# Kernel optimization log

Measured on AMD Instinct MI355X. Metric: run time of the kernel, lower is better.

Reference implementation:

```python
import jax, jax.numpy as jnp
import numpy as np

H = 8      # n_heads
HD = 64    # per-head channels (out_channels in __init__, before *= n_heads)


def setup_inputs() -> dict:
    key = jax.random.key(0)
    ks = jax.random.split(key, 10)
    B, C, N = 4, 256, 2048
    O = H * HD
    s = 1.0 / np.sqrt(C).astype(np.float32)
    return {
        "x": jax.random.normal(ks[0], (B, C, N), dtype=jnp.float32),
        "y": jax.random.normal(ks[1], (B, C, N), dtype=jnp.float32),
        "Wq": jax.random.normal(ks[2], (O, C), dtype=jnp.float32) * s,
        "bq": jnp.zeros((O,), dtype=jnp.float32),
        "Wk": jax.random.normal(ks[3], (O, C), dtype=jnp.float32) * s,
        "bk": jnp.zeros((O,), dtype=jnp.float32),
        "Wv": jax.random.normal(ks[4], (O, C), dtype=jnp.float32) * s,
        "bv": jnp.zeros((O,), dtype=jnp.float32),
        "Wp": jax.random.normal(ks[5], (HD, C), dtype=jnp.float32) * s,  # residual projection, bias=False
        "gamma": jax.random.uniform(ks[6], (H, 1, 1, 1), dtype=jnp.float32) + 0.001,
    }


def _conv1x1(W, b, t):
    # 1x1 Conv1d: (O,C) x (B,C,N) -> (B,O,N)
    out = jnp.einsum('oc,bcn->bon', W, t)
    return out if b is None else out + b[None, :, None]


def _heads(t):
    # (B, H*HD, N) -> (H, B, N, HD); channel split into contiguous per-head chunks
    B, _, N = t.shape
    return t.reshape(B, H, HD, N).transpose(1, 0, 3, 2)


def reference(x, y, Wq, bq, Wk, bk, Wv, bv, Wp, gamma):
    # q/k/v projections via 1x1 convs (kernel_size=1, 'stride_effective' padding => same length)
    q = _heads(_conv1x1(Wq, bq, x))   # (H,B,N,HD)
    k = _heads(_conv1x1(Wk, bk, y))   # (H,B,N,HD)
    v = _heads(_conv1x1(Wv, bv, y))   # (H,B,N,HD)

    # energy = bmm(Q, K^T); softmax over last dim (no mask)
    energy = jnp.einsum('hbnd,hbmd->hbnm', q, k)          # (H,B,N,N)
    attn = jax.nn.softmax(energy, axis=-1)

    # out = bmm(attention.transpose(-2,-1), V)  (note the transpose in the original)
    out = jnp.einsum('hbnm,hbnd->hbmd', attn, v)          # (H,B,N,HD)

    # gamma-weighted residual blend with projected y
    yp = _conv1x1(Wp, None, y).transpose(0, 2, 1)         # (B,N,HD)
    g = gamma.reshape(H, 1, 1, 1)
    out = (g * out + yp[None]) / (1.0 + g)                # (H,B,N,HD)
    return out
```

## Files before the change

### kernel.cpp

```cpp
#include <hip/hip_runtime.h>
#include <math.h>

#define B_DIM 4
#define C_DIM 256
#define N_DIM 2048
#define H_DIM 8
#define HD    64
#define HB    32
#define NTOK  (B_DIM * N_DIM)
#define LOG2E 1.44269504f

typedef __attribute__((ext_vector_type(8))) short bf16x8;
typedef __attribute__((ext_vector_type(4))) float f32x4;

static __device__ __forceinline__ short f2bf(float f) {
    unsigned u = __builtin_bit_cast(unsigned, f);
    u += 0x7fffu + ((u >> 16) & 1u);
    return (short)(u >> 16);
}
static __device__ __forceinline__ float bf2f(short s) {
    unsigned u = ((unsigned)(unsigned short)s) << 16;
    return __builtin_bit_cast(float, u);
}
static __device__ __forceinline__ float fx2(float x) {
#if __has_builtin(__builtin_amdgcn_exp2f)
    return __builtin_amdgcn_exp2f(x);
#else
    return exp2f(x);
#endif
}
static __device__ __forceinline__ unsigned pk_bf16(float a, float b) {
#if __has_builtin(__builtin_amdgcn_cvt_pk_bf16_f32)
    auto v = __builtin_amdgcn_cvt_pk_bf16_f32(a, b);
    return __builtin_bit_cast(unsigned, v);
#else
    unsigned ua = __builtin_bit_cast(unsigned, a);
    unsigned ub = __builtin_bit_cast(unsigned, b);
    return ((ua + 0x8000u) >> 16) | ((ub + 0x8000u) & 0xffff0000u);
#endif
}

#define MFMA16(A, Bv, Cv) __builtin_amdgcn_mfma_f32_16x16x32_bf16(A, Bv, Cv, 0, 0, 0)


__global__ __launch_bounds__(256) void cast_transpose_xy(
    const float* __restrict__ X, const float* __restrict__ Y,
    short* __restrict__ XS, short* __restrict__ YS)
{
    const int z = blockIdx.z;
    const float* src = (z < 4) ? X : Y;
    short* dst = (z < 4) ? XS : YS;
    const int b = z & 3, c0 = blockIdx.y * 64, n0 = blockIdx.x * 64;
    __shared__ float L[64][65];
    const int t = threadIdx.x;
    for (int i = t; i < 4096; i += 256) {
        int cc = i >> 6, nn = i & 63;
        L[cc][nn] = src[((size_t)b * C_DIM + c0 + cc) * N_DIM + n0 + nn];
    }
    __syncthreads();
#pragma unroll
    for (int half = 0; half < 2; ++half) {
        int cid = half * 256 + t;
        int lane = cid & 63, fi = cid >> 6;
        int ksl = fi & 1, rtl = fi >> 1;
        int lo = lane & 15, quad = lane >> 4;
        bf16x8 o;
#pragma unroll
        for (int j = 0; j < 8; ++j) o[j] = f2bf(L[ksl * 32 + quad * 8 + j][rtl * 16 + lo]);
        int rt = b * 128 + (n0 >> 4) + rtl;
        int ks = (c0 >> 5) + ksl;
        *(bf16x8*)(dst + ((size_t)(rt * 8 + ks) * 64 + lane) * 8) = o;
    }
}

__global__ __launch_bounds__(256) void cast_weights(
    const float* __restrict__ Wq, const float* __restrict__ Wk,
    const float* __restrict__ Wv, const float* __restrict__ Wp,
    short* __restrict__ WSx, short* __restrict__ WSy)
{
    int gid = blockIdx.x * 256 + threadIdx.x;
    int lane = gid & 63, chunk = gid >> 6;
    int lo = lane & 15, quad = lane >> 4;
    const float* src; short* dst;
    if (chunk < 256) {
        int ot = chunk >> 3, ks = chunk & 7;
        src = Wq + (size_t)(ot * 16 + lo) * C_DIM + ks * 32 + quad * 8;
        dst = WSx + (size_t)chunk * 512 + lane * 8;
    } else {
        int ch = chunk - 256;
        int ot = ch >> 3, ks = ch & 7;
        int row = ot * 16 + lo;
        const float* base = (row < 512) ? (Wk + (size_t)row * C_DIM)
                          : (row < 1024) ? (Wv + (size_t)(row - 512) * C_DIM)
                                         : (Wp + (size_t)(row - 1024) * C_DIM);
        src = base + ks * 32 + quad * 8;
        dst = WSy + (size_t)ch * 512 + lane * 8;
    }
    bf16x8 o;
#pragma unroll
    for (int j = 0; j < 8; ++j) o[j] = f2bf(src[j]);
    *(bf16x8*)dst = o;
}

__global__ __launch_bounds__(256) void proj_all(
    const short* __restrict__ WSx, const short* __restrict__ WSy,
    const short* __restrict__ XS, const short* __restrict__ YS,
    const float* __restrict__ bq, const float* __restrict__ bk,
    const float* __restrict__ bv,
    short* __restrict__ QS, short* __restrict__ KS,
    short* __restrict__ VSu, float* __restrict__ Yo)
{
    const int oy = blockIdx.y;
    const bool isq = oy < 8;
    const short* WS = isq ? WSx : WSy;
    const short* Xs = isq ? XS : YS;
    const int oyl = isq ? oy : oy - 8;
    const int o0 = oyl * 64;
    const int tok0 = blockIdx.x * 128;
    const int t = threadIdx.x, wave = t >> 6, lane = t & 63;
    const int lo = lane & 15, quad = lane >> 4;

    __shared__ __align__(16) char smem[34816];

    const int ot = oyl * 4 + wave;
    const int rt0 = tok0 >> 4;
    const f32x4 czero = {0.f, 0.f, 0.f, 0.f};

    f32x4 acc[8];
#pragma unroll
    for (int i = 0; i < 8; ++i) acc[i] = czero;

#pragma unroll 2
    for (int ks = 0; ks < 8; ++ks) {
        bf16x8 a = *(const bf16x8*)(WS + ((size_t)(ot * 8 + ks) * 64 + lane) * 8);
#pragma unroll
        for (int nt = 0; nt < 8; ++nt) {
            bf16x8 bx = *(const bf16x8*)(Xs + ((size_t)((rt0 + nt) * 8 + ks) * 64 + lane) * 8);
            acc[nt] = MFMA16(a, bx, acc[nt]);
        }
    }

    const int b = tok0 >> 11;
    const int n0b = tok0 & (N_DIM - 1);

    if (oy < 16) {
        short* T = (short*)smem;
        const float* bias = isq ? bq : bk;
        const float scale = isq ? LOG2E : 1.f;
        float bvr[4];
#pragma unroll
        for (int r = 0; r < 4; ++r) bvr[r] = bias[o0 + wave * 16 + quad * 4 + r];
#pragma unroll
        for (int nt = 0; nt < 8; ++nt) {
            short4 pk;
            pk.x = f2bf((acc[nt][0] + bvr[0]) * scale);
            pk.y = f2bf((acc[nt][1] + bvr[1]) * scale);
            pk.z = f2bf((acc[nt][2] + bvr[2]) * scale);
            pk.w = f2bf((acc[nt][3] + bvr[3]) * scale);
            *(short4*)(T + (nt * 16 + lo) * 72 + wave * 16 + quad * 4) = pk;
        }
        __syncthreads();
        const int h = oyl;
        const int hb = h * 4 + b;
        short* dst = isq ? QS : KS;
#pragma unroll
        for (int s = 0; s < 4; ++s) {
            int cid = s * 256 + t;
            int ln = cid & 63, fi = cid >> 6;
            int ksd = fi & 1, rtl = fi >> 1;
            bf16x8 v = *(const bf16x8*)(T + (rtl * 16 + (ln & 15)) * 72 + ksd * 32 + (ln >> 4) * 8);
            *(bf16x8*)(dst + (((size_t)(hb * 128 + (n0b >> 4) + rtl) * 2 + ksd) * 512 + ln * 8)) = v;
        }
    } else if (oy < 24) {
        short* T2 = (short*)smem;
        float bvr[4];
#pragma unroll
        for (int r = 0; r < 4; ++r) bvr[r] = bv[o0 - 512 + wave * 16 + quad * 4 + r];
#pragma unroll
        for (int nt = 0; nt < 8; ++nt)
#pragma unroll
            for (int r = 0; r < 4; ++r) {
                int ol = wave * 16 + quad * 4 + r;
                T2[ol * 136 + nt * 16 + lo] = f2bf(acc[nt][r] + bvr[r]);
            }
        __syncthreads();
        const int h = oy - 16;
        const int hb = h * 4 + b;
#pragma unroll
        for (int s = 0; s < 4; ++s) {
            int cid = s * 256 + t;
            int ln = cid & 63, fi = cid >> 6;
            int dt = fi & 3, ksd = (fi >> 2) & 1, nbl = fi >> 3;
            int dl = dt * 16 + (ln & 15);
            int tkl = nbl * 64 + ksd * 32 + (ln >> 4) * 8;
            bf16x8 v = *(const bf16x8*)(T2 + dl * 136 + tkl);
            int nbg = (n0b >> 6) + nbl;
            *(bf16x8*)(VSu + ((size_t)(((hb * 32 + nbg) * 2 + ksd) * 4 + dt) * 64 + ln) * 8) = v;
        }
    } else {
        float* T3 = (float*)smem;
#pragma unroll
        for (int nt = 0; nt < 8; ++nt) {
            float4 f;
            f.x = acc[nt][0]; f.y = acc[nt][1]; f.z = acc[nt][2]; f.w = acc[nt][3];
            *(float4*)(T3 + (nt * 16 + lo) * 68 + wave * 16 + quad * 4) = f;
        }
        __syncthreads();
#pragma unroll
        for (int s = 0; s < 8; ++s) {
            int cid = s * 256 + t;
            int row = cid >> 4, c4 = (cid & 15) * 4;
            float4 f = *(const float4*)(T3 + row * 68 + c4);
            *(float4*)(Yo + ((size_t)(tok0 + row)) * 64 + c4) = f;
        }
    }
}

__global__ __launch_bounds__(256, 4) void rowsum_mfma(
    const short* __restrict__ QS, const short* __restrict__ KS,
    float* __restrict__ RSp)
{
    const int id = blockIdx.x;
    const int hb = ((id & 7) << 2) | ((id >> 3) & 3);
    const int z = (id >> 5) & 1;
    const int n0 = (id >> 6) * 128;
    const int t = threadIdx.x, wave = t >> 6, lane = t & 63;
    const int lo = lane & 15, quad = lane >> 4;
    const f32x4 czero = {0.f, 0.f, 0.f, 0.f};

    bf16x8 a0[2], a1[2];
#pragma unroll
    for (int s = 0; s < 2; ++s) {
        int rt = (n0 >> 4) + s * 4 + wave;
        a0[s] = *(const bf16x8*)(QS + ((size_t)(hb * 128 + rt) * 2 + 0) * 512 + lane * 8);
        a1[s] = *(const bf16x8*)(QS + ((size_t)(hb * 128 + rt) * 2 + 1) * 512 + lane * 8);
    }

    float sm[2][4];
#pragma unroll
    for (int s = 0; s < 2; ++s)
#pragma unroll
        for (int r = 0; r < 4; ++r) sm[s][r] = 0.f;

    const short* kp = KS + ((size_t)(hb * 128) * 2) * 512 + lane * 8
                    + (size_t)z * (N_DIM / 2 / 16) * 2 * 512;
    for (int m0 = 0; m0 < N_DIM / 2; m0 += 64) {
#pragma unroll
        for (int mt = 0; mt < 4; ++mt) {
            bf16x8 b0 = *(const bf16x8*)(kp + (mt * 2 + 0) * 512);
            bf16x8 b1 = *(const bf16x8*)(kp + (mt * 2 + 1) * 512);
#pragma unroll
            for (int s = 0; s < 2; ++s) {
                f32x4 c = MFMA16(a0[s], b0, czero);
                c = MFMA16(a1[s], b1, c);
#pragma unroll
                for (int r = 0; r < 4; ++r) sm[s][r] += fx2(c[r]);
            }
        }
        kp += 8 * 512;
    }

#pragma unroll
    for (int sft = 1; sft < 16; sft <<= 1)
#pragma unroll
        for (int s = 0; s < 2; ++s)
#pragma unroll
            for (int r = 0; r < 4; ++r) sm[s][r] += __shfl_xor(sm[s][r], sft);

    if (lo == 0) {
#pragma unroll
        for (int s = 0; s < 2; ++s) {
            int row = n0 + s * 64 + wave * 16 + quad * 4;
#pragma unroll
            for (int r = 0; r < 4; ++r)
                RSp[((size_t)z * HB + hb) * N_DIM + row + r] = sm[s][r];
        }
    }
}

__global__ __launch_bounds__(256) void v_scale(
    const short* __restrict__ VSu, const float* __restrict__ RSp,
    short* __restrict__ VS)
{
    int t = blockIdx.x * 256 + threadIdx.x;
    int lane = t & 63, fidx = t >> 6;
    int ks = (fidx >> 2) & 1, nb = (fidx >> 3) & 31, hb = fidx >> 8;
    int n = nb * 64 + ks * 32 + (lane >> 4) * 8;
    bf16x8 v = *(const bf16x8*)(VSu + (size_t)t * 8);
    const float* r0 = RSp + (size_t)hb * N_DIM + n;
    const float* r1 = r0 + (size_t)HB * N_DIM;
    bf16x8 o;
#pragma unroll
    for (int j = 0; j < 8; ++j) o[j] = f2bf(bf2f(v[j]) / (r0[j] + r1[j]));
    *(bf16x8*)(VS + (size_t)t * 8) = o;
}

__global__ __launch_bounds__(256, 4) void attnout_mfma(
    const short* __restrict__ QS, const short* __restrict__ KS,
    const short* __restrict__ VS,
    short* __restrict__ PA0, short* __restrict__ PA1)
{
    const int id = blockIdx.x;
    const int hb = ((id & 7) << 2) | ((id >> 3) & 3);
    const int z = (id >> 5) & 1;
    const int m0 = (id >> 6) * 128;

    __shared__ __align__(16) char smem[17408];
    short* Pl = (short*)smem;

    const int t = threadIdx.x, wave = t >> 6, lane = t & 63;
    const int lo = lane & 15, quad = lane >> 4;
    const f32x4 czero = {0.f, 0.f, 0.f, 0.f};

    bf16x8 bk0[2], bk1[2];
#pragma unroll
    for (int s = 0; s < 2; ++s) {
        int rt = (m0 >> 4) + s * 4 + wave;
        bk0[s] = *(const bf16x8*)(KS + ((size_t)(hb * 128 + rt) * 2 + 0) * 512 + lane * 8);
        bk1[s] = *(const bf16x8*)(KS + ((size_t)(hb * 128 + rt) * 2 + 1) * 512 + lane * 8);
    }

    f32x4 oacc[2][4];
#pragma unroll
    for (int s = 0; s < 2; ++s)
#pragma unroll
        for (int dt = 0; dt < 4; ++dt) oacc[s][dt] = czero;

    const short* qp = QS + ((size_t)(hb * 128) * 2) * 512 + lane * 8
                    + (size_t)z * (N_DIM / 2 / 16) * 2 * 512;
    const short* vp = VS + ((size_t)(hb * 32) * 8) * 512 + lane * 8
                    + (size_t)z * (N_DIM / 2 / 64) * 8 * 512;
    short* prowA = Pl + (wave * 16 + lo) * 64;
    short* prowB = prowA + 64 * 64;
    const int lh = lo & 7;

    for (int n0 = 0; n0 < N_DIM / 2; n0 += 64) {
#pragma unroll
        for (int nt = 0; nt < 4; ++nt) {
            bf16x8 a0 = *(const bf16x8*)(qp + (nt * 2 + 0) * 512);
            bf16x8 a1 = *(const bf16x8*)(qp + (nt * 2 + 1) * 512);
#pragma unroll
            for (int s = 0; s < 2; ++s) {
                f32x4 c = MFMA16(a0, bk0[s], czero);
                c = MFMA16(a1, bk1[s], c);
                uint2 pk;
                pk.x = pk_bf16(fx2(c[0]), fx2(c[1]));
                pk.y = pk_bf16(fx2(c[2]), fx2(c[3]));
                int chunk = nt * 2 + (quad >> 1);
                *(uint2*)((s ? prowB : prowA) + (((chunk ^ lh) << 3) | ((quad & 1) << 2))) = pk;
            }
        }
#pragma unroll
        for (int ks = 0; ks < 2; ++ks) {
            bf16x8 ap0 = *(const bf16x8*)(prowA + (((ks * 4 + quad) ^ lh) << 3));
            bf16x8 ap1 = *(const bf16x8*)(prowB + (((ks * 4 + quad) ^ lh) << 3));
#pragma unroll
            for (int dt = 0; dt < 4; ++dt) {
                bf16x8 bv = *(const bf16x8*)(vp + (ks * 4 + dt) * 512);
                oacc[0][dt] = MFMA16(ap0, bv, oacc[0][dt]);
                oacc[1][dt] = MFMA16(ap1, bv, oacc[1][dt]);
            }
        }
        qp += 8 * 512;
        vp += 8 * 512;
    }

    short* PA = z ? PA1 : PA0;
    float* T = (float*)smem;
#pragma unroll
    for (int s = 0; s < 2; ++s) {
        __syncthreads();
#pragma unroll
        for (int dt = 0; dt < 4; ++dt)
#pragma unroll
            for (int r = 0; r < 4; ++r)
                T[(wave * 16 + quad * 4 + r) * 68 + dt * 16 + lo] = oacc[s][dt][r];
        __syncthreads();
#pragma unroll
        for (int it = 0; it < 2; ++it) {
            int idx = it * 256 + t;
            int rowl = idx >> 3, dg = (idx & 7) * 8;
            float4 f0 = *(const float4*)(T + rowl * 68 + dg);
            float4 f1 = *(const float4*)(T + rowl * 68 + dg + 4);
            uint4 o;
            o.x = pk_bf16(f0.x, f0.y);
            o.y = pk_bf16(f0.z, f0.w);
            o.z = pk_bf16(f1.x, f1.y);
            o.w = pk_bf16(f1.z, f1.w);
            int m = m0 + s * 64 + rowl;
            *(uint4*)(PA + ((size_t)(hb * N_DIM + m)) * 64 + dg) = o;
        }
    }
}

__global__ __launch_bounds__(256) void combine_out(
    const short* __restrict__ PA0, const short* __restrict__ PA1,
    const float* __restrict__ YP, const float* __restrict__ gamma,
    float* __restrict__ out)
{
    size_t flat = ((size_t)blockIdx.x * 256 + threadIdx.x) * 8;
    int d  = (int)(flat & 63);
    int n  = (int)((flat >> 6) & (N_DIM - 1));
    int hb = (int)(flat >> 17);
    int h = hb >> 2, b = hb & 3;
    float g = gamma[h];
    float inv = 1.f / (1.f + g);
    float gi = g * inv;
    bf16x8 p0 = *(const bf16x8*)(PA0 + flat);
    bf16x8 p1 = *(const bf16x8*)(PA1 + flat);
    const float* yp = YP + ((size_t)b * N_DIM + n) * HD + d;
    float o[8];
#pragma unroll
    for (int j = 0; j < 8; ++j)
        o[j] = gi * (bf2f(p0[j]) + bf2f(p1[j])) + inv * yp[j];
    float4 o0 = {o[0], o[1], o[2], o[3]};
    float4 o1 = {o[4], o[5], o[6], o[7]};
    *(float4*)(out + flat) = o0;
    *(float4*)(out + flat + 4) = o1;
}

extern "C" void kernel_launch(void* const* d_in, const int* in_sizes, int n_in,
                              void* d_out, int out_size, void* d_ws, size_t ws_size,
                              hipStream_t stream) {
    const float* x     = (const float*)d_in[0];
    const float* y     = (const float*)d_in[1];
    const float* Wq    = (const float*)d_in[2];
    const float* bq    = (const float*)d_in[3];
    const float* Wk    = (const float*)d_in[4];
    const float* bk    = (const float*)d_in[5];
    const float* Wv    = (const float*)d_in[6];
    const float* bv    = (const float*)d_in[7];
    const float* Wp    = (const float*)d_in[8];
    const float* gamma = (const float*)d_in[9];
    float* out = (float*)d_out;

    const size_t XEL  = (size_t)B_DIM * C_DIM * N_DIM;
    const size_t QKV  = (size_t)HB * N_DIM * HD;

    short* XS  = (short*)d_ws;
    short* YS  = XS + XEL;
    short* WSx = YS + XEL;
    short* WSy = WSx + 512 * C_DIM;
    short* QS  = WSy + 1088 * C_DIM;
    short* KS  = QS + QKV;
    short* VSu = KS + QKV;
    short* VS  = VSu + QKV;
    float* YPb = (float*)(VS + QKV);
    float* RSp = YPb + (size_t)B_DIM * N_DIM * HD;
    short* PA0 = XS;
    short* PA1 = VSu;

    dim3 blk(256);
    cast_transpose_xy<<<dim3(N_DIM / 64, C_DIM / 64, 8), blk, 0, stream>>>(x, y, XS, YS);
    cast_weights<<<dim3(200), blk, 0, stream>>>(Wq, Wk, Wv, Wp, WSx, WSy);

    proj_all<<<dim3(NTOK / 128, 25), blk, 0, stream>>>(
        WSx, WSy, XS, YS, bq, bk, bv, QS, KS, VSu, YPb);

    rowsum_mfma<<<dim3(1024), blk, 0, stream>>>(QS, KS, RSp);
    v_scale<<<dim3(2048), blk, 0, stream>>>(VSu, RSp, VS);
    attnout_mfma<<<dim3(1024), blk, 0, stream>>>(QS, KS, VS, PA0, PA1);
    combine_out<<<dim3(2048), blk, 0, stream>>>(PA0, PA1, YPb, gamma, out);
}
```

Before: 192.7 us.

## Software-pipeline QK^T MFMAs ahead of PV in attention loop; merge cast kernels

The attention-output loop is software-pipelined. The QK^T MFMAs for the next 64-column tile are issued while the current tile's exp/pack to LDS and the PV MFMAs are in flight, with a prologue and epilogue around the loop. The Q fragment loads are also hoisted to the start of each iteration. Separately, the weight-cast kernel is folded into the x/y cast-transpose kernel as an extra z-slice, which removes one launch. The pipelining raises register pressure because eight accumulators plus the prefetched A fragments stay live, which could lower occupancy.

Measured after the change: 186.4 us. 3.2% less time.

```diff
diff --git a/kernel.cpp b/kernel.cpp
--- a/kernel.cpp
+++ b/kernel.cpp
@@ -43,16 +43,51 @@
 #define MFMA16(A, Bv, Cv) __builtin_amdgcn_mfma_f32_16x16x32_bf16(A, Bv, Cv, 0, 0, 0)
 
 
-__global__ __launch_bounds__(256) void cast_transpose_xy(
+__global__ __launch_bounds__(256) void cast_all(
     const float* __restrict__ X, const float* __restrict__ Y,
-    short* __restrict__ XS, short* __restrict__ YS)
+    const float* __restrict__ Wq, const float* __restrict__ Wk,
+    const float* __restrict__ Wv, const float* __restrict__ Wp,
+    short* __restrict__ XS, short* __restrict__ YS,
+    short* __restrict__ WSx, short* __restrict__ WSy)
 {
     const int z = blockIdx.z;
+    const int t = threadIdx.x;
+
+    if (z == 8) {
+        int base = (blockIdx.y * 32 + blockIdx.x) * 256 + t;
+#pragma unroll
+        for (int rep = 0; rep < 2; ++rep) {
+            int gid = base + rep * 32768;
+            if (gid >= 51200) break;
+            int lane = gid & 63, chunk = gid >> 6;
+            int lo = lane & 15, quad = lane >> 4;
+            const float* src; short* dst;
+            if (chunk < 256) {
+                int ot = chunk >> 3, ks = chunk & 7;
+                src = Wq + (size_t)(ot * 16 + lo) * C_DIM + ks * 32 + quad * 8;
+                dst = WSx + (size_t)chunk * 512 + lane * 8;
+            } else {
+                int ch = chunk - 256;
+                int ot = ch >> 3, ks = ch & 7;
+                int row = ot * 16 + lo;
+                const float* basep = (row < 512) ? (Wk + (size_t)row * C_DIM)
+                                   : (row < 1024) ? (Wv + (size_t)(row - 512) * C_DIM)
+                                                  : (Wp + (size_t)(row - 1024) * C_DIM);
+                src = basep + ks * 32 + quad * 8;
+                dst = WSy + (size_t)ch * 512 + lane * 8;
+            }
+            bf16x8 o;
+#pragma unroll
+            for (int j = 0; j < 8; ++j) o[j] = f2bf(src[j]);
+            *(bf16x8*)dst = o;
+        }
+        return;
+    }
+
     const float* src = (z < 4) ? X : Y;
     short* dst = (z < 4) ? XS : YS;
     const int b = z & 3, c0 = blockIdx.y * 64, n0 = blockIdx.x * 64;
     __shared__ float L[64][65];
-    const int t = threadIdx.x;
     for (int i = t; i < 4096; i += 256) {
         int cc = i >> 6, nn = i & 63;
         L[cc][nn] = src[((size_t)b * C_DIM + c0 + cc) * N_DIM + n0 + nn];
@@ -71,35 +106,6 @@
         int ks = (c0 >> 5) + ksl;
         *(bf16x8*)(dst + ((size_t)(rt * 8 + ks) * 64 + lane) * 8) = o;
     }
-}
-
-__global__ __launch_bounds__(256) void cast_weights(
-    const float* __restrict__ Wq, const float* __restrict__ Wk,
-    const float* __restrict__ Wv, const float* __restrict__ Wp,
-    short* __restrict__ WSx, short* __restrict__ WSy)
-{
-    int gid = blockIdx.x * 256 + threadIdx.x;
-    int lane = gid & 63, chunk = gid >> 6;
-    int lo = lane & 15, quad = lane >> 4;
-    const float* src; short* dst;
-    if (chunk < 256) {
-        int ot = chunk >> 3, ks = chunk & 7;
-        src = Wq + (size_t)(ot * 16 + lo) * C_DIM + ks * 32 + quad * 8;
-        dst = WSx + (size_t)chunk * 512 + lane * 8;
-    } else {
-        int ch = chunk - 256;
-        int ot = ch >> 3, ks = ch & 7;
-        int row = ot * 16 + lo;
-        const float* base = (row < 512) ? (Wk + (size_t)row * C_DIM)
-                          : (row < 1024) ? (Wv + (size_t)(row - 512) * C_DIM)
-                                         : (Wp + (size_t)(row - 1024) * C_DIM);
-        src = base + ks * 32 + quad * 8;
-        dst = WSy + (size_t)ch * 512 + lane * 8;
-    }
-    bf16x8 o;
-#pragma unroll
-    for (int j = 0; j < 8; ++j) o[j] = f2bf(src[j]);
-    *(bf16x8*)dst = o;
 }
 
 __global__ __launch_bounds__(256) void proj_all(
@@ -333,23 +339,48 @@
     short* prowA = Pl + (wave * 16 + lo) * 64;
     short* prowB = prowA + 64 * 64;
     const int lh = lo & 7;
-
-    for (int n0 = 0; n0 < N_DIM / 2; n0 += 64) {
+    const int NIT = N_DIM / 2 / 64;
+
+    f32x4 c[4][2];
+
+    {
 #pragma unroll
         for (int nt = 0; nt < 4; ++nt) {
             bf16x8 a0 = *(const bf16x8*)(qp + (nt * 2 + 0) * 512);
             bf16x8 a1 = *(const bf16x8*)(qp + (nt * 2 + 1) * 512);
 #pragma unroll
             for (int s = 0; s < 2; ++s) {
-                f32x4 c = MFMA16(a0, bk0[s], czero);
-                c = MFMA16(a1, bk1[s], c);
+                c[nt][s] = MFMA16(a0, bk0[s], czero);
+                c[nt][s] = MFMA16(a1, bk1[s], c[nt][s]);
+            }
+        }
+        qp += 8 * 512;
+    }
+
+    for (int i = 0; i < NIT - 1; ++i) {
+        bf16x8 a0[4], a1[4];
+#pragma unroll
+        for (int nt = 0; nt < 4; ++nt) {
+            a0[nt] = *(const bf16x8*)(qp + (nt * 2 + 0) * 512);
+            a1[nt] = *(const bf16x8*)(qp + (nt * 2 + 1) * 512);
+        }
+#pragma unroll
+        for (int nt = 0; nt < 4; ++nt)
+#pragma unroll
+            for (int s = 0; s < 2; ++s) {
                 uint2 pk;
-                pk.x = pk_bf16(fx2(c[0]), fx2(c[1]));
-                pk.y = pk_bf16(fx2(c[2]), fx2(c[3]));
+                pk.x = pk_bf16(fx2(c[nt][s][0]), fx2(c[nt][s][1]));
+                pk.y = pk_bf16(fx2(c[nt][s][2]), fx2(c[nt][s][3]));
                 int chunk = nt * 2 + (quad >> 1);
                 *(uint2*)((s ? prowB : prowA) + (((chunk ^ lh) << 3) | ((quad & 1) << 2))) = pk;
             }
-        }
+#pragma unroll
+        for (int nt = 0; nt < 4; ++nt)
+#pragma unroll
+            for (int s = 0; s < 2; ++s) {
+                c[nt][s] = MFMA16(a0[nt], bk0[s], czero);
+                c[nt][s] = MFMA16(a1[nt], bk1[s], c[nt][s]);
+            }
 #pragma unroll
         for (int ks = 0; ks < 2; ++ks) {
             bf16x8 ap0 = *(const bf16x8*)(prowA + (((ks * 4 + quad) ^ lh) << 3));
@@ -363,6 +394,28 @@
         }
         qp += 8 * 512;
         vp += 8 * 512;
+    }
+
+#pragma unroll
+    for (int nt = 0; nt < 4; ++nt)
+#pragma unroll
+        for (int s = 0; s < 2; ++s) {
+            uint2 pk;
+            pk.x = pk_bf16(fx2(c[nt][s][0]), fx2(c[nt][s][1]));
+            pk.y = pk_bf16(fx2(c[nt][s][2]), fx2(c[nt][s][3]));
+            int chunk = nt * 2 + (quad >> 1);
+            *(uint2*)((s ? prowB : prowA) + (((chunk ^ lh) << 3) | ((quad & 1) << 2))) = pk;
+        }
+#pragma unroll
+    for (int ks = 0; ks < 2; ++ks) {
+        bf16x8 ap0 = *(const bf16x8*)(prowA + (((ks * 4 + quad) ^ lh) << 3));
+        bf16x8 ap1 = *(const bf16x8*)(prowB + (((ks * 4 + quad) ^ lh) << 3));
+#pragma unroll
+        for (int dt = 0; dt < 4; ++dt) {
+            bf16x8 bv = *(const bf16x8*)(vp + (ks * 4 + dt) * 512);
+            oacc[0][dt] = MFMA16(ap0, bv, oacc[0][dt]);
+            oacc[1][dt] = MFMA16(ap1, bv, oacc[1][dt]);
+        }
     }
 
     short* PA = z ? PA1 : PA0;
@@ -451,8 +504,8 @@
     short* PA1 = VSu;
 
     dim3 blk(256);
-    cast_transpose_xy<<<dim3(N_DIM / 64, C_DIM / 64, 8), blk, 0, stream>>>(x, y, XS, YS);
-    cast_weights<<<dim3(200), blk, 0, stream>>>(Wq, Wk, Wv, Wp, WSx, WSy);
+    cast_all<<<dim3(N_DIM / 64, C_DIM / 64, 9), blk, 0, stream>>>(
+        x, y, Wq, Wk, Wv, Wp, XS, YS, WSx, WSy);
 
     proj_all<<<dim3(NTOK / 128, 25), blk, 0, stream>>>(
         WSx, WSy, XS, YS, bq, bk, bv, QS, KS, VSu, YPb);
```
